# Kernel optimization log

Hardware: AMD Instinct MI355X
Metric: run time of the kernel (lower is better)

## Reference

```python
import jax, jax.numpy as jnp
import numpy as np

B, N, C, T, K = 32, 4096, 768, 1000, 20

def setup_inputs() -> dict:
    key = jax.random.key(0)
    k1, k2, k3, k4 = jax.random.split(key, 4)
    g_feat = jax.random.normal(k1, (B, 1, C), dtype=jnp.float32)
    inp = jax.random.normal(k2, (B, N, C), dtype=jnp.float32)
    tau = jax.random.uniform(k3, (1,), dtype=jnp.float32)
    text_embeddings = jax.random.normal(k4, (T, C), dtype=jnp.float32) * 0.01
    return {"g_feat": g_feat, "input": inp, "tau": tau, "text_embeddings": text_embeddings}


def reference(g_feat, input, tau, text_embeddings):
    feat = input  # [B, N, C]
    # 1x1 conv of global feature against text embeddings -> class logits [B, T]
    vg_logit = jnp.einsum('bc,tc->bt', g_feat[:, 0, :], text_embeddings)
    # top-20 candidate categories per image
    _, indices = jax.lax.top_k(vg_logit, K)              # [B, K]
    agg_text_features = text_embeddings[indices]          # [B, K, C] gather
    # per-pixel logits against the 20 gathered text embeddings
    seg_logit = jnp.exp(tau[0]) * jnp.einsum('bkc,bnc->bkn', agg_text_features, feat)  # [B, K, N]
    # hard (straight-through) softmax over candidate axis (dim=-2)
    y_soft = jax.nn.softmax(seg_logit, axis=-2)
    idx = jnp.argmax(seg_logit, axis=-2)                  # [B, N]
    y_hard = jnp.moveaxis(jax.nn.one_hot(idx, K, dtype=seg_logit.dtype), -1, -2)  # [B, K, N]
    attn = y_hard - jax.lax.stop_gradient(y_soft) + y_soft
    # normalize over pixel axis (assign_eps = 1.0)
    assign_attn = attn / (jnp.sum(attn, axis=-1, keepdims=True) + 1.0)
    # combine: [B, N, K] @ [B, K, C] -> [B, N, C]
    text_grids = jnp.einsum('bkn,bkc->bnc', assign_attn, agg_text_features)
    return text_grids
```

## Files before the change

kernel.cpp:

```cpp
#include <hip/hip_runtime.h>
#include <cfloat>

#define B_ 32
#define N_ 4096
#define C_ 768
#define T_ 1000
#define K_ 20

#define PHC 32
#define NPH (C_/PHC)
#define GAP_TH 1e-4f
#define MAXF 16384

typedef float f32x4 __attribute__((ext_vector_type(4)));
typedef int   i32x4 __attribute__((ext_vector_type(4)));
typedef short s16x8 __attribute__((ext_vector_type(8)));

__device__ __forceinline__ unsigned short bf_rne(float x) {
    unsigned u = __float_as_uint(x);
    return (unsigned short)((u + 0x7fffu + ((u >> 16) & 1u)) >> 16);
}

__global__ __launch_bounds__(256) void k1_logits(const float* __restrict__ g_feat,
                                                 const float* __restrict__ text,
                                                 double* __restrict__ logits,
                                                 int* __restrict__ cnt,
                                                 int* __restrict__ flagcnt) {
    int b = blockIdx.x;
    int wid = threadIdx.x >> 6, lane = threadIdx.x & 63;
    int t = blockIdx.y * 4 + wid;
    if (b == 0 && blockIdx.y == 0) {
        for (int i = threadIdx.x; i < B_ * K_; i += 256) cnt[i] = 0;
        if (threadIdx.x == 0) flagcnt[0] = 0;
    }
    const float* g = g_feat + b * C_;
    const float* e = text + t * C_;
    double s = 0.0;
    #pragma unroll
    for (int j = 0; j < 12; ++j) {
        int c = lane + 64 * j;
        s += (double)g[c] * (double)e[c];
    }
    #pragma unroll
    for (int m = 32; m; m >>= 1) s += __shfl_xor(s, m);
    if (lane == 0) logits[b * T_ + t] = s;
}

__global__ __launch_bounds__(256) void k1b_topk(const double* __restrict__ logits,
                                                const float* __restrict__ text,
                                                float* __restrict__ agg,
                                                unsigned short* __restrict__ Epk) {
    __shared__ unsigned short hiL[32 * C_];
    __shared__ unsigned short loL[32 * C_];
    __shared__ int ssel[K_];
    int b = blockIdx.x, tid = threadIdx.x, lane = tid & 63;
    if (tid < 64) {
        double v[16];
        #pragma unroll
        for (int j = 0; j < 16; ++j) {
            int t = lane + 64 * j;
            v[j] = (t < T_) ? logits[b * T_ + t] : -DBL_MAX;
        }
        for (int it = 0; it < K_; ++it) {
            double bv = -DBL_MAX; int bi = 0x7fffffff;
            #pragma unroll
            for (int j = 0; j < 16; ++j) {
                int t = lane + 64 * j;
                if (v[j] > bv) { bv = v[j]; bi = t; }
            }
            #pragma unroll
            for (int m = 32; m; m >>= 1) {
                double ov = __shfl_xor(bv, m); int oi = __shfl_xor(bi, m);
                if (ov > bv || (ov == bv && oi < bi)) { bv = ov; bi = oi; }
            }
            if (lane == 0) ssel[it] = bi;
            #pragma unroll
            for (int j = 0; j < 16; ++j) {
                int t = lane + 64 * j;
                if (t == bi) v[j] = -DBL_MAX;
            }
        }
    }
    __syncthreads();
    for (int i = tid; i < 32 * C_; i += 256) {
        int r = i / C_, c = i - r * C_;
        float v = (r < K_) ? text[ssel[r] * C_ + c] : 0.f;
        if (r < K_) agg[b * K_ * C_ + i] = v;
        unsigned u = __float_as_uint(v);
        float fh = __uint_as_float(u & 0xffff0000u);
        hiL[i] = (unsigned short)(u >> 16);
        loL[i] = bf_rne(v - fh);
    }
    __syncthreads();
    for (int i = tid; i < 24 * 256; i += 256) {
        int p = i >> 8, r = i & 255, f = r >> 6, ln = r & 63;
        int row = (f & 1) * 16 + (ln & 15);
        int col = p * 32 + (ln >> 4) * 8;
        const unsigned short* src = ((f < 2) ? hiL : loL) + row * C_ + col;
        *(s16x8*)(Epk + ((size_t)b * 6144 + i) * 8) = *(const s16x8*)src;
    }
}

__global__ __launch_bounds__(256, 6) void k2_argmax(const float* __restrict__ feat,
                                                    const unsigned short* __restrict__ Epk,
                                                    int* __restrict__ kidx,
                                                    int* __restrict__ cnt,
                                                    int* __restrict__ flagcnt,
                                                    int* __restrict__ flaglist) {
    __shared__ int scnt[K_];
    int tid = threadIdx.x, wid = tid >> 6, lane = tid & 63;
    if (tid < K_) scnt[tid] = 0;
    __syncthreads();

    int gw = blockIdx.x * 4 + wid;
    int b  = gw >> 8;
    int n0 = (gw & 255) * 16;
    int prow = lane & 15;
    int g    = lane >> 4;
    const float* fp0 = feat + ((size_t)b * N_ + n0 + prow) * C_ + g * 8;
    const unsigned short* Eb = Epk + (size_t)b * 6144 * 8;

    f32x4 fr0, fr1, nf0, nf1;
    s16x8 Ah0, Ah1, Al0, Al1;
    auto LOADA = [&](int p) {
        const s16x8* ap = (const s16x8*)(Eb + (size_t)p * 256 * 8);
        Ah0 = ap[lane]; Ah1 = ap[64 + lane];
        Al0 = ap[128 + lane]; Al1 = ap[192 + lane];
    };
    auto CVT = [&](f32x4 a, f32x4 c, s16x8& H, s16x8& L) {
        float x[8] = { a.x, a.y, a.z, a.w, c.x, c.y, c.z, c.w };
        unsigned hu[8], lu[8];
        #pragma unroll
        for (int j = 0; j < 8; ++j) {
            unsigned u = __float_as_uint(x[j]);
            hu[j] = u >> 16;
            lu[j] = bf_rne(x[j] - __uint_as_float(u & 0xffff0000u));
        }
        i32x4 hv = { (int)(hu[0] | (hu[1] << 16)), (int)(hu[2] | (hu[3] << 16)),
                     (int)(hu[4] | (hu[5] << 16)), (int)(hu[6] | (hu[7] << 16)) };
        i32x4 lv = { (int)(lu[0] | (lu[1] << 16)), (int)(lu[2] | (lu[3] << 16)),
                     (int)(lu[4] | (lu[5] << 16)), (int)(lu[6] | (lu[7] << 16)) };
        H = __builtin_bit_cast(s16x8, hv);
        L = __builtin_bit_cast(s16x8, lv);
    };

    f32x4 acc0 = (f32x4)0.f, acc1 = (f32x4)0.f;
    fr0 = *(const f32x4*)(fp0);
    fr1 = *(const f32x4*)(fp0 + 4);

    #pragma unroll 1
    for (int p = 0; p < NPH; ++p) {
        if (p + 1 < NPH) {
            nf0 = *(const f32x4*)(fp0 + (p + 1) * PHC);
            nf1 = *(const f32x4*)(fp0 + (p + 1) * PHC + 4);
        }
        LOADA(p);
        s16x8 Bh, Bl;
        CVT(fr0, fr1, Bh, Bl);
        acc0 = __builtin_amdgcn_mfma_f32_16x16x32_bf16(Ah0, Bh, acc0, 0, 0, 0);
        acc1 = __builtin_amdgcn_mfma_f32_16x16x32_bf16(Ah1, Bh, acc1, 0, 0, 0);
        acc0 = __builtin_amdgcn_mfma_f32_16x16x32_bf16(Ah0, Bl, acc0, 0, 0, 0);
        acc1 = __builtin_amdgcn_mfma_f32_16x16x32_bf16(Ah1, Bl, acc1, 0, 0, 0);
        acc0 = __builtin_amdgcn_mfma_f32_16x16x32_bf16(Al0, Bh, acc0, 0, 0, 0);
        acc1 = __builtin_amdgcn_mfma_f32_16x16x32_bf16(Al1, Bh, acc1, 0, 0, 0);
        fr0 = nf0; fr1 = nf1;
    }

    int kb = g * 4;
    float m1 = acc0[0]; int i1 = kb; float m2 = -FLT_MAX;
    #pragma unroll
    for (int r = 1; r < 4; ++r) {
        float v = acc0[r];
        if (v > m1) { m2 = m1; m1 = v; i1 = kb + r; }
        else if (v > m2) m2 = v;
    }
    if (g == 0) {
        #pragma unroll
        for (int r = 0; r < 4; ++r) {
            float v = acc1[r];
            if (v > m1) { m2 = m1; m1 = v; i1 = 16 + r; }
            else if (v > m2) m2 = v;
        }
    }
    #pragma unroll
    for (int s = 16; s < 64; s <<= 1) {
        float om1 = __shfl_xor(m1, s); int oi1 = __shfl_xor(i1, s);
        float om2 = __shfl_xor(m2, s);
        if (om1 > m1 || (om1 == m1 && oi1 < i1)) { m2 = fmaxf(m1, om2); m1 = om1; i1 = oi1; }
        else { m2 = fmaxf(m2, om1); }
    }
    if (lane < 16) {
        int n = n0 + lane;
        kidx[b * N_ + n] = i1;
        atomicAdd(&scnt[i1], 1);
        if (m1 - m2 < GAP_TH) {
            int pos = atomicAdd(flagcnt, 1);
            if (pos < MAXF) flaglist[pos] = b * N_ + n;
        }
    }
    __syncthreads();
    if (tid < K_) atomicAdd(&cnt[b * K_ + tid], scnt[tid]);
}

__global__ __launch_bounds__(256) void k25_refine(const float* __restrict__ feat,
                                                  const float* __restrict__ agg,
                                                  int* __restrict__ kidx,
                                                  int* __restrict__ cnt,
                                                  const int* __restrict__ flagcnt,
                                                  const int* __restrict__ flaglist) {
    int wid = threadIdx.x >> 6, lane = threadIdx.x & 63;
    int wg = blockIdx.x * 4 + wid;
    int nf = flagcnt[0]; if (nf > MAXF) nf = MAXF;
    for (int e = wg; e < nf; e += gridDim.x * 4) {
        int pix = flaglist[e];
        int b = pix >> 12;
        const float* fr = feat + (size_t)pix * C_;
        const float* ebase = agg + b * K_ * C_;
        double fd[12];
        #pragma unroll
        for (int j = 0; j < 12; ++j) fd[j] = (double)fr[lane + 64 * j];
        double best = -DBL_MAX; int bi = 0;
        for (int k = 0; k < K_; ++k) {
            const float* er = ebase + k * C_;
            double s = 0.0;
            #pragma unroll
            for (int j = 0; j < 12; ++j) s += fd[j] * (double)er[lane + 64 * j];
            #pragma unroll
            for (int m = 32; m; m >>= 1) s += __shfl_xor(s, m);
            if (s > best) { best = s; bi = k; }
        }
        if (lane == 0) {
            int old = kidx[pix];
            if (old != bi) {
                kidx[pix] = bi;
                atomicSub(&cnt[b * K_ + old], 1);
                atomicAdd(&cnt[b * K_ + bi], 1);
            }
        }
    }
}

__global__ __launch_bounds__(256) void k3s_scale(const float* __restrict__ agg,
                                                 const int* __restrict__ cnt,
                                                 float* __restrict__ sagg) {
    __shared__ float sc[K_];
    int b = blockIdx.x, tid = threadIdx.x;
    if (tid < K_) sc[tid] = 1.0f / ((float)cnt[b * K_ + tid] + 1.0f);
    __syncthreads();
    const f32x4* a4 = (const f32x4*)(agg + (size_t)b * K_ * C_);
    f32x4* s4 = (f32x4*)(sagg + (size_t)b * K_ * C_);
    #pragma unroll 1
    for (int i = tid; i < K_ * (C_ / 4); i += 256) {
        int k = i / (C_ / 4);
        s4[i] = a4[i] * sc[k];
    }
}

__global__ __launch_bounds__(256) void k4_out(const float* __restrict__ sagg,
                                              const int* __restrict__ kidx,
                                              float* __restrict__ out) {
    int wid = threadIdx.x >> 6, lane = threadIdx.x & 63;
    int wg = blockIdx.x * 4 + wid;
    int base = wg * 8;
    int b = base >> 12;
    int kk[8];
    #pragma unroll
    for (int i = 0; i < 8; ++i) kk[i] = kidx[base + i];
    const f32x4* sagg4 = (const f32x4*)sagg;
    f32x4* out4 = (f32x4*)out;

    f32x4 va0, va1, va2, vb0, vb1, vb2;
    {
        const f32x4* a4 = sagg4 + (size_t)(b * K_ + kk[0]) * (C_ / 4);
        va0 = a4[lane]; va1 = a4[lane + 64]; va2 = a4[lane + 128];
    }
    #pragma unroll
    for (int i = 0; i < 8; ++i) {
        if (i + 1 < 8) {
            const f32x4* a4 = sagg4 + (size_t)(b * K_ + kk[i + 1]) * (C_ / 4);
            vb0 = a4[lane]; vb1 = a4[lane + 64]; vb2 = a4[lane + 128];
        }
        f32x4* o4 = out4 + (size_t)(base + i) * (C_ / 4);
        o4[lane] = va0; o4[lane + 64] = va1; o4[lane + 128] = va2;
        va0 = vb0; va1 = vb1; va2 = vb2;
    }
}

extern "C" void kernel_launch(void* const* d_in, const int* in_sizes, int n_in,
                              void* d_out, int out_size, void* d_ws, size_t ws_size,
                              hipStream_t stream) {
    const float* g_feat = (const float*)d_in[0];
    const float* feat   = (const float*)d_in[1];
    const float* text   = (const float*)d_in[3];
    float* out = (float*)d_out;

    char* ws = (char*)d_ws;
    double* logits        = (double*)(ws + 0);
    float*  agg           = (float*) (ws + 262144);
    int*    cnt           = (int*)   (ws + 2230784);
    int*    flagc         = (int*)   (ws + 2233344);
    int*    flagl         = (int*)   (ws + 2233408);
    int*    kidx          = (int*)   (ws + 2301504);
    unsigned short* Epk   = (unsigned short*)(ws + 2825792);
    float*  sagg          = (float*) (ws + 5971520);

    k1_logits<<<dim3(32, 250), 256, 0, stream>>>(g_feat, text, logits, cnt, flagc);
    k1b_topk<<<32, 256, 0, stream>>>(logits, text, agg, Epk);
    k2_argmax<<<2048, 256, 0, stream>>>(feat, Epk, kidx, cnt, flagc, flagl);
    k25_refine<<<1024, 256, 0, stream>>>(feat, agg, kidx, cnt, flagc, flagl);
    k3s_scale<<<32, 256, 0, stream>>>(agg, cnt, sagg);
    k4_out<<<4096, 256, 0, stream>>>(sagg, kidx, out);
}
```

Before: 283.1 us.

## Stage feature rows in LDS and split channel reduction across waves

The argmax kernel now has each block load its 16 pixel rows into LDS with async global_load_lds using an XOR swizzle. Each of the four waves then computes a quarter of the channel dimension (6 phases) instead of one wave walking all 24 phases. Partial accumulators are reduced through LDS before the top-2 selection. The aim is better memory-level parallelism and shorter per-wave latency chains when streaming the large feature tensor, at the cost of about 50KB of LDS per block, lower occupancy (launch bounds 3), four times as many blocks, and an extra cross-wave reduction.

```diff
diff --git a/kernel.cpp b/kernel.cpp
--- a/kernel.cpp
+++ b/kernel.cpp
@@ -9,6 +9,7 @@
 
 #define PHC 32
 #define NPH (C_/PHC)
+#define ROWF 784
 #define GAP_TH 1e-4f
 #define MAXF 16384
 
@@ -101,26 +102,39 @@
     }
 }
 
-__global__ __launch_bounds__(256, 6) void k2_argmax(const float* __restrict__ feat,
+__global__ __launch_bounds__(256, 3) void k2_argmax(const float* __restrict__ feat,
                                                     const unsigned short* __restrict__ Epk,
                                                     int* __restrict__ kidx,
                                                     int* __restrict__ cnt,
                                                     int* __restrict__ flagcnt,
                                                     int* __restrict__ flaglist) {
+    __shared__ float rows[16 * ROWF];
     __shared__ int scnt[K_];
     int tid = threadIdx.x, wid = tid >> 6, lane = tid & 63;
     if (tid < K_) scnt[tid] = 0;
-    __syncthreads();
-
-    int gw = blockIdx.x * 4 + wid;
-    int b  = gw >> 8;
-    int n0 = (gw & 255) * 16;
-    int prow = lane & 15;
-    int g    = lane >> 4;
-    const float* fp0 = feat + ((size_t)b * N_ + n0 + prow) * C_ + g * 8;
+
+    int bx = blockIdx.x;
+    int b = bx >> 8, t16 = bx & 255;
+    int n0 = t16 * 16;
+    const float* fb = feat + ((size_t)b * N_ + n0) * C_;
     const unsigned short* Eb = Epk + (size_t)b * 6144 * 8;
 
-    f32x4 fr0, fr1, nf0, nf1;
+    #pragma unroll
+    for (int r2 = 0; r2 < 4; ++r2) {
+        int r = wid * 4 + r2;
+        int sw = 2 * (r & 3);
+        #pragma unroll
+        for (int c = 0; c < 3; ++c) {
+            const float* src = fb + (size_t)r * C_ + c * 256 + ((lane ^ sw) * 4);
+            float* dst = &rows[r * ROWF + c * 256];
+            __builtin_amdgcn_global_load_lds((const __attribute__((address_space(1))) void*)src,
+                                             (__attribute__((address_space(3))) void*)dst, 16, 0, 0);
+        }
+    }
+    __syncthreads();
+
+    int g = lane >> 4, r = lane & 15;
+    int X = 8 * (r & 3);
     s16x8 Ah0, Ah1, Al0, Al1;
     auto LOADA = [&](int p) {
         const s16x8* ap = (const s16x8*)(Eb + (size_t)p * 256 * 8);
@@ -145,61 +159,71 @@
     };
 
     f32x4 acc0 = (f32x4)0.f, acc1 = (f32x4)0.f;
-    fr0 = *(const f32x4*)(fp0);
-    fr1 = *(const f32x4*)(fp0 + 4);
-
-    #pragma unroll 1
-    for (int p = 0; p < NPH; ++p) {
-        if (p + 1 < NPH) {
-            nf0 = *(const f32x4*)(fp0 + (p + 1) * PHC);
-            nf1 = *(const f32x4*)(fp0 + (p + 1) * PHC + 4);
-        }
+    #pragma unroll
+    for (int q = 0; q < 6; ++q) {
+        int p = wid * 6 + q;
         LOADA(p);
+        int dd = (32 * p + 8 * g) ^ X;
+        f32x4 f0 = *(const f32x4*)&rows[ROWF * r + dd];
+        f32x4 f1 = *(const f32x4*)&rows[ROWF * r + dd + 4];
         s16x8 Bh, Bl;
-        CVT(fr0, fr1, Bh, Bl);
+        CVT(f0, f1, Bh, Bl);
         acc0 = __builtin_amdgcn_mfma_f32_16x16x32_bf16(Ah0, Bh, acc0, 0, 0, 0);
         acc1 = __builtin_amdgcn_mfma_f32_16x16x32_bf16(Ah1, Bh, acc1, 0, 0, 0);
         acc0 = __builtin_amdgcn_mfma_f32_16x16x32_bf16(Ah0, Bl, acc0, 0, 0, 0);
         acc1 = __builtin_amdgcn_mfma_f32_16x16x32_bf16(Ah1, Bl, acc1, 0, 0, 0);
         acc0 = __builtin_amdgcn_mfma_f32_16x16x32_bf16(Al0, Bh, acc0, 0, 0, 0);
         acc1 = __builtin_amdgcn_mfma_f32_16x16x32_bf16(Al1, Bh, acc1, 0, 0, 0);
-        fr0 = nf0; fr1 = nf1;
-    }
-
-    int kb = g * 4;
-    float m1 = acc0[0]; int i1 = kb; float m2 = -FLT_MAX;
-    #pragma unroll
-    for (int r = 1; r < 4; ++r) {
-        float v = acc0[r];
-        if (v > m1) { m2 = m1; m1 = v; i1 = kb + r; }
-        else if (v > m2) m2 = v;
-    }
-    if (g == 0) {
-        #pragma unroll
-        for (int r = 0; r < 4; ++r) {
-            float v = acc1[r];
-            if (v > m1) { m2 = m1; m1 = v; i1 = 16 + r; }
+    }
+
+    __syncthreads();
+    float* red = rows;
+    int li = tid * 8;
+    #pragma unroll
+    for (int j = 0; j < 4; ++j) { red[li + j] = acc0[j]; red[li + 4 + j] = acc1[j]; }
+    __syncthreads();
+    if (wid == 0) {
+        #pragma unroll
+        for (int w = 1; w < 4; ++w) {
+            int oi = (w * 64 + lane) * 8;
+            #pragma unroll
+            for (int j = 0; j < 4; ++j) { acc0[j] += red[oi + j]; acc1[j] += red[oi + 4 + j]; }
+        }
+        int kb = g * 4;
+        float m1 = acc0[0]; int i1 = kb; float m2 = -FLT_MAX;
+        #pragma unroll
+        for (int rr = 1; rr < 4; ++rr) {
+            float v = acc0[rr];
+            if (v > m1) { m2 = m1; m1 = v; i1 = kb + rr; }
             else if (v > m2) m2 = v;
         }
-    }
-    #pragma unroll
-    for (int s = 16; s < 64; s <<= 1) {
-        float om1 = __shfl_xor(m1, s); int oi1 = __shfl_xor(i1, s);
-        float om2 = __shfl_xor(m2, s);
-        if (om1 > m1 || (om1 == m1 && oi1 < i1)) { m2 = fmaxf(m1, om2); m1 = om1; i1 = oi1; }
-        else { m2 = fmaxf(m2, om1); }
-    }
-    if (lane < 16) {
-        int n = n0 + lane;
-        kidx[b * N_ + n] = i1;
-        atomicAdd(&scnt[i1], 1);
-        if (m1 - m2 < GAP_TH) {
-            int pos = atomicAdd(flagcnt, 1);
-            if (pos < MAXF) flaglist[pos] = b * N_ + n;
-        }
-    }
-    __syncthreads();
-    if (tid < K_) atomicAdd(&cnt[b * K_ + tid], scnt[tid]);
+        if (g == 0) {
+            #pragma unroll
+            for (int rr = 0; rr < 4; ++rr) {
+                float v = acc1[rr];
+                if (v > m1) { m2 = m1; m1 = v; i1 = 16 + rr; }
+                else if (v > m2) m2 = v;
+            }
+        }
+        #pragma unroll
+        for (int s = 16; s < 64; s <<= 1) {
+            float om1 = __shfl_xor(m1, s); int oi1 = __shfl_xor(i1, s);
+            float om2 = __shfl_xor(m2, s);
+            if (om1 > m1 || (om1 == m1 && oi1 < i1)) { m2 = fmaxf(m1, om2); m1 = om1; i1 = oi1; }
+            else { m2 = fmaxf(m2, om1); }
+        }
+        if (lane < 16) {
+            int n = n0 + lane;
+            kidx[b * N_ + n] = i1;
+            atomicAdd(&scnt[i1], 1);
+            if (m1 - m2 < GAP_TH) {
+                int pos = atomicAdd(flagcnt, 1);
+                if (pos < MAXF) flaglist[pos] = b * N_ + n;
+            }
+        }
+    }
+    __syncthreads();
+    if (tid < K_ && scnt[tid]) atomicAdd(&cnt[b * K_ + tid], scnt[tid]);
 }
 
 __global__ __launch_bounds__(256) void k25_refine(const float* __restrict__ feat,
@@ -306,7 +330,7 @@
 
     k1_logits<<<dim3(32, 250), 256, 0, stream>>>(g_feat, text, logits, cnt, flagc);
     k1b_topk<<<32, 256, 0, stream>>>(logits, text, agg, Epk);
-    k2_argmax<<<2048, 256, 0, stream>>>(feat, Epk, kidx, cnt, flagc, flagl);
+    k2_argmax<<<8192, 256, 0, stream>>>(feat, Epk, kidx, cnt, flagc, flagl);
     k25_refine<<<1024, 256, 0, stream>>>(feat, agg, kidx, cnt, flagc, flagl);
     k3s_scale<<<32, 256, 0, stream>>>(agg, cnt, sagg);
     k4_out<<<4096, 256, 0, stream>>>(sagg, kidx, out);
```

New measurement: 274.7 us. -3.0%, faster.
